# Kernel tuning notes

Hardware: AMD Instinct MI355X
Metric: run time of the kernel (lower is better)

The kernel has to match this reference:

```python
import jax, jax.numpy as jnp
import numpy as np


def _ln(x, g, b, eps=1e-5):
    m = x.mean(-1, keepdims=True)
    v = x.var(-1, keepdims=True)
    return (x - m) / jnp.sqrt(v + eps) * g + b


def setup_inputs() -> dict:
    key = jax.random.key(0)
    ks = jax.random.split(key, 10)
    N, H, E, OUT, L = 4096, 256, 131072, 64, 6
    s = 1.0 / np.sqrt(H)
    return {
        "x": jax.random.normal(ks[0], (N, H), jnp.float32),
        "edge_index": jax.random.randint(ks[1], (2, E), 0, N, jnp.int32),
        "sage_wl": jax.random.normal(ks[2], (L, H, H), jnp.float32) * s,   # lin_l (neighbors, has bias)
        "sage_wr": jax.random.normal(ks[3], (L, H, H), jnp.float32) * s,   # lin_r (root, no bias)
        "sage_bl": jnp.zeros((L, H), jnp.float32),
        "ln_g": jnp.ones((L - 1, H), jnp.float32),
        "ln_b": jnp.zeros((L - 1, H), jnp.float32),
        "conv_w": jax.random.normal(ks[4], (3, H, H, 3), jnp.float32) * (1.0 / np.sqrt(3 * H)),  # [layer,O,I,K]
        "conv_b": jnp.zeros((3, H), jnp.float32),
        "cnorm_g": jnp.ones((3, H), jnp.float32),
        "cnorm_b": jnp.zeros((3, H), jnp.float32),
        "in_proj_w": jax.random.normal(ks[5], (6 * H, 2 * H), jnp.float32) * (1.0 / np.sqrt(2 * H)),
        "in_proj_b": jnp.zeros((6 * H,), jnp.float32),
        "out_proj_w": jax.random.normal(ks[6], (2 * H, 2 * H), jnp.float32) * (1.0 / np.sqrt(2 * H)),
        "out_proj_b": jnp.zeros((2 * H,), jnp.float32),
        "anorm_g": jnp.ones((2 * H,), jnp.float32),
        "anorm_b": jnp.zeros((2 * H,), jnp.float32),
        "fuse_w": jax.random.normal(ks[7], (OUT, 2 * H), jnp.float32) * (1.0 / np.sqrt(2 * H)),
        "fuse_b": jnp.zeros((OUT,), jnp.float32),
    }


def reference(x, edge_index, sage_wl, sage_wr, sage_bl, ln_g, ln_b,
              conv_w, conv_b, cnorm_g, cnorm_b,
              in_proj_w, in_proj_b, out_proj_w, out_proj_b,
              anorm_g, anorm_b, fuse_w, fuse_b):
    # Dropout layers act as identity (eval mode).
    N, H = x.shape
    L = sage_wl.shape[0]
    src, dst = edge_index[0], edge_index[1]
    deg = jax.ops.segment_sum(jnp.ones(src.shape[0], x.dtype), dst, num_segments=N)
    deg = jnp.maximum(deg, 1.0)[:, None]
    h = x
    for i in range(L):
        res = h
        # SAGEConv: mean-aggregate neighbor features (gather/scatter), then two linears
        agg = jax.ops.segment_sum(h[src], dst, num_segments=N) / deg
        h = agg @ sage_wl[i].T + sage_bl[i] + h @ sage_wr[i].T
        if i < L - 1:
            h = _ln(h, ln_g[i], ln_b[i])
        h = jax.nn.relu(h) + res  # residual (shapes always match: in==hidden)
    gnn_out = h                                   # [N, H]

    # CNN branch over the node axis: [1, H, N]
    c = gnn_out.T[None]
    for j in range(3):
        c = jax.lax.conv_general_dilated(c, conv_w[j], (1,), ((1, 1),),
                                         dimension_numbers=("NCH", "OIH", "NCH"))
        c = jax.nn.relu(c + conv_b[j][None, :, None])
        c = _ln(c.transpose(0, 2, 1), cnorm_g[j], cnorm_b[j]).transpose(0, 2, 1)
    cnn_out = c[0].T                              # [N, H]

    fused = jnp.concatenate([gnn_out, cnn_out], axis=1)  # [N, 2H]
    E2 = fused.shape[1]
    heads = 4
    hd = E2 // heads
    qkv = fused @ in_proj_w.T + in_proj_b
    q, k, v = jnp.split(qkv, 3, axis=1)
    split_heads = lambda t: t.reshape(N, heads, hd).transpose(1, 0, 2)  # [h, N, hd]
    q, k, v = split_heads(q), split_heads(k), split_heads(v)
    scores = jnp.einsum("hnd,hmd->hnm", q, k) / np.sqrt(hd).astype(np.float32)
    a = jax.nn.softmax(scores, axis=-1)
    o = jnp.einsum("hnm,hmd->hnd", a, v).transpose(1, 0, 2).reshape(N, E2)
    o = o @ out_proj_w.T + out_proj_b
    o = _ln(o, anorm_g, anorm_b)
    return o @ fuse_w.T + fuse_b                  # [N, out_channels]
```

## Files before the change

### kernel.cpp

```cpp
#include <hip/hip_runtime.h>

#define NN 4096
#define HH 256
#define EE 131072

__device__ __constant__ float LN_EPS = 1e-5f;
#define ATT_SCALE 0.08838834764831845f
#define ATT_SHIFT 30.0f

typedef __attribute__((ext_vector_type(8))) short bf16x8_t;
typedef __attribute__((ext_vector_type(4))) float f32x4_t;

__device__ inline ushort f2b(float f) {
  uint u = __float_as_uint(f);
  uint r = (u + 0x7FFF + ((u >> 16) & 1)) >> 16;
  return (ushort)r;
}

__global__ void hist_kernel(const int* __restrict__ ei, int* __restrict__ cnt) {
  int e = blockIdx.x * blockDim.x + threadIdx.x;
  if (e < EE) atomicAdd(&cnt[ei[EE + e]], 1);
}

__global__ __launch_bounds__(1024) void scan_kernel(int* __restrict__ cnt_cursor,
                                                    int* __restrict__ rowptr,
                                                    float* __restrict__ invdeg) {
  __shared__ int part[1024];
  int t = threadIdx.x;
  int base = t * 4;
  int cs[4];
  int s = 0;
  for (int u = 0; u < 4; ++u) { cs[u] = cnt_cursor[base + u]; s += cs[u]; }
  part[t] = s;
  __syncthreads();
  for (int off = 1; off < 1024; off <<= 1) {
    int add = (t >= off) ? part[t - off] : 0;
    int v = part[t];
    __syncthreads();
    part[t] = v + add;
    __syncthreads();
  }
  int excl = (t > 0) ? part[t - 1] : 0;
  for (int u = 0; u < 4; ++u) {
    rowptr[base + u] = excl;
    cnt_cursor[base + u] = excl;
    invdeg[base + u] = 1.0f / (float)max(cs[u], 1);
    excl += cs[u];
  }
  if (t == 1023) rowptr[NN] = excl;
}

__global__ void fill_kernel(const int* __restrict__ ei, int* __restrict__ cursor,
                            int* __restrict__ col) {
  int e = blockIdx.x * blockDim.x + threadIdx.x;
  if (e < EE) {
    int d = ei[EE + e];
    int p = atomicAdd(&cursor[d], 1);
    col[p] = ei[e];
  }
}

__global__ __launch_bounds__(256) void castw(const float* __restrict__ in,
                                             ushort* __restrict__ out) {
  int i4 = (blockIdx.x * 256 + threadIdx.x) * 4;
  float4 v = *(const float4*)(in + i4);
  ushort4 w;
  w.x = f2b(v.x); w.y = f2b(v.y); w.z = f2b(v.z); w.w = f2b(v.w);
  *(ushort4*)(out + i4) = w;
}

__global__ __launch_bounds__(256) void castconv(const float* __restrict__ w,
                                                ushort* __restrict__ o) {
  int idx = blockIdx.x * 256 + threadIdx.x;
  int j = idx / 196608;
  int rem = idx - j * 196608;
  int oc = rem / 768;
  int kk = rem - oc * 768;
  int ks = kk >> 8, ii = kk & 255;
  o[idx] = f2b(w[j * 196608 + oc * 768 + ii * 3 + ks]);
}

__global__ __launch_bounds__(64) void agg_kernel(const float* __restrict__ h,
                                                 const int* __restrict__ rowptr,
                                                 const int* __restrict__ col,
                                                 const float* __restrict__ invdeg,
                                                 ushort* __restrict__ aggb) {
  int n = blockIdx.x;
  int t = threadIdx.x;
  int s = rowptr[n], e = rowptr[n + 1];
  float4 acc = make_float4(0.f, 0.f, 0.f, 0.f);
  for (int j = s; j < e; ++j) {
    int c = col[j];
    const float4 v = *(const float4*)(h + (size_t)c * HH + t * 4);
    acc.x += v.x; acc.y += v.y; acc.z += v.z; acc.w += v.w;
  }
  float id = invdeg[n];
  ushort4 w;
  w.x = f2b(acc.x * id); w.y = f2b(acc.y * id);
  w.z = f2b(acc.z * id); w.w = f2b(acc.w * id);
  *(ushort4*)(aggb + (size_t)n * HH + t * 4) = w;
}

__global__ __launch_bounds__(256) void gemm_mfma(
    const ushort* __restrict__ A0, const ushort* __restrict__ A1,
    const ushort* __restrict__ B0, const ushort* __restrict__ B1,
    const float* __restrict__ bias, float* __restrict__ Cf, ushort* __restrict__ Cb,
    int M, int Nn, int K, int KHA, int KHB, int relu) {
  __shared__ ushort Alds[64][40];
  __shared__ ushort Blds[128][40];
  int t = threadIdx.x;
  int w = t >> 6, l = t & 63, quad = l >> 4, lr = l & 15;
  int wm = w & 1, wn = w >> 1;
  int m0 = blockIdx.x * 64, n0 = blockIdx.y * 128;
  int sr = t >> 2, sc8 = (t & 3) * 8;
  f32x4_t acc[2][4];
#pragma unroll
  for (int s = 0; s < 2; ++s)
#pragma unroll
    for (int q = 0; q < 4; ++q) acc[s][q] = (f32x4_t){0.f, 0.f, 0.f, 0.f};

  for (int k0 = 0; k0 < K; k0 += 32) {
    int kk = k0 + sc8;
    const ushort* ap = (kk < KHA) ? (A0 + (size_t)(m0 + sr) * KHA + kk)
                                  : (A1 + (size_t)(m0 + sr) * (K - KHA) + (kk - KHA));
    uint4 av = *(const uint4*)ap;
    const ushort* bp0 = (kk < KHB) ? (B0 + (size_t)(n0 + sr) * KHB + kk)
                                   : (B1 + (size_t)(n0 + sr) * (K - KHB) + (kk - KHB));
    uint4 bv0 = *(const uint4*)bp0;
    const ushort* bp1 = (kk < KHB) ? (B0 + (size_t)(n0 + 64 + sr) * KHB + kk)
                                   : (B1 + (size_t)(n0 + 64 + sr) * (K - KHB) + (kk - KHB));
    uint4 bv1 = *(const uint4*)bp1;
    __syncthreads();
    *(uint4*)&Alds[sr][sc8] = av;
    *(uint4*)&Blds[sr][sc8] = bv0;
    *(uint4*)&Blds[64 + sr][sc8] = bv1;
    __syncthreads();
    bf16x8_t af[2], bf[4];
#pragma unroll
    for (int s = 0; s < 2; ++s)
      af[s] = *(const bf16x8_t*)&Alds[wm * 32 + s * 16 + lr][quad * 8];
#pragma unroll
    for (int q = 0; q < 4; ++q)
      bf[q] = *(const bf16x8_t*)&Blds[wn * 64 + q * 16 + lr][quad * 8];
#pragma unroll
    for (int s = 0; s < 2; ++s)
#pragma unroll
      for (int q = 0; q < 4; ++q)
        acc[s][q] = __builtin_amdgcn_mfma_f32_16x16x32_bf16(af[s], bf[q], acc[s][q], 0, 0, 0);
  }
#pragma unroll
  for (int s = 0; s < 2; ++s) {
#pragma unroll
    for (int q = 0; q < 4; ++q) {
      int n = n0 + wn * 64 + q * 16 + lr;
      float bb = bias[n];
#pragma unroll
      for (int r = 0; r < 4; ++r) {
        int m = m0 + wm * 32 + s * 16 + quad * 4 + r;
        float v = acc[s][q][r] + bb;
        if (relu) v = fmaxf(v, 0.f);
        if (Cf) Cf[(size_t)m * Nn + n] = v;
        if (Cb) Cb[(size_t)m * Nn + n] = f2b(v);
      }
    }
  }
}

__global__ __launch_bounds__(256) void gemm_conv_mfma(
    const ushort* __restrict__ Ab, const ushort* __restrict__ B,
    const float* __restrict__ bias, float* __restrict__ Cf) {
  __shared__ ushort Alds[64][40];
  __shared__ ushort Blds[128][40];
  int t = threadIdx.x;
  int w = t >> 6, l = t & 63, quad = l >> 4, lr = l & 15;
  int wm = w & 1, wn = w >> 1;
  int m0 = blockIdx.x * 64, n0 = blockIdx.y * 128;
  int sr = t >> 2, sc8 = (t & 3) * 8;
  f32x4_t acc[2][4];
#pragma unroll
  for (int s = 0; s < 2; ++s)
#pragma unroll
    for (int q = 0; q < 4; ++q) acc[s][q] = (f32x4_t){0.f, 0.f, 0.f, 0.f};

  for (int k0 = 0; k0 < 768; k0 += 32) {
    int kk = k0 + sc8;
    int ks = kk >> 8, ii = kk & 255;
    int nr = m0 + sr + ks - 1;
    uint4 av = make_uint4(0u, 0u, 0u, 0u);
    if (nr >= 0 && nr < NN) av = *(const uint4*)(Ab + (size_t)nr * HH + ii);
    uint4 bv0 = *(const uint4*)(B + (size_t)(n0 + sr) * 768 + kk);
    uint4 bv1 = *(const uint4*)(B + (size_t)(n0 + 64 + sr) * 768 + kk);
    __syncthreads();
    *(uint4*)&Alds[sr][sc8] = av;
    *(uint4*)&Blds[sr][sc8] = bv0;
    *(uint4*)&Blds[64 + sr][sc8] = bv1;
    __syncthreads();
    bf16x8_t af[2], bf[4];
#pragma unroll
    for (int s = 0; s < 2; ++s)
      af[s] = *(const bf16x8_t*)&Alds[wm * 32 + s * 16 + lr][quad * 8];
#pragma unroll
    for (int q = 0; q < 4; ++q)
      bf[q] = *(const bf16x8_t*)&Blds[wn * 64 + q * 16 + lr][quad * 8];
#pragma unroll
    for (int s = 0; s < 2; ++s)
#pragma unroll
      for (int q = 0; q < 4; ++q)
        acc[s][q] = __builtin_amdgcn_mfma_f32_16x16x32_bf16(af[s], bf[q], acc[s][q], 0, 0, 0);
  }
#pragma unroll
  for (int s = 0; s < 2; ++s) {
#pragma unroll
    for (int q = 0; q < 4; ++q) {
      int n = n0 + wn * 64 + q * 16 + lr;
      float bb = bias[n];
#pragma unroll
      for (int r = 0; r < 4; ++r) {
        int m = m0 + wm * 32 + s * 16 + quad * 4 + r;
        Cf[(size_t)m * HH + n] = fmaxf(acc[s][q][r] + bb, 0.f);
      }
    }
  }
}

__global__ __launch_bounds__(256) void gemm_std(
    const float* __restrict__ A0, const float* __restrict__ B0,
    const float* __restrict__ bias, float* __restrict__ C,
    int M, int Nn, int K) {
  __shared__ float As[16][68];
  __shared__ float Bs[16][68];
  int t = threadIdx.x;
  int m0 = blockIdx.x * 64, n0 = blockIdx.y * 64;
  int ty = t >> 4, tx = t & 15;
  int lr = t >> 2, lc4 = (t & 3) * 4;
  float acc[4][4] = {};
  for (int k0 = 0; k0 < K; k0 += 16) {
    int kk = k0 + lc4;
    float4 va = *(const float4*)(A0 + (size_t)(m0 + lr) * K + kk);
    As[lc4 + 0][lr] = va.x; As[lc4 + 1][lr] = va.y;
    As[lc4 + 2][lr] = va.z; As[lc4 + 3][lr] = va.w;
    float4 vb = *(const float4*)(B0 + (size_t)(n0 + lr) * K + kk);
    Bs[lc4 + 0][lr] = vb.x; Bs[lc4 + 1][lr] = vb.y;
    Bs[lc4 + 2][lr] = vb.z; Bs[lc4 + 3][lr] = vb.w;
    __syncthreads();
#pragma unroll
    for (int k = 0; k < 16; ++k) {
      float4 a4 = *(const float4*)&As[k][4 * ty];
      float4 b4 = *(const float4*)&Bs[k][4 * tx];
      float av[4] = {a4.x, a4.y, a4.z, a4.w};
      float bv[4] = {b4.x, b4.y, b4.z, b4.w};
#pragma unroll
      for (int i = 0; i < 4; ++i)
#pragma unroll
        for (int j = 0; j < 4; ++j) acc[i][j] += av[i] * bv[j];
    }
    __syncthreads();
  }
#pragma unroll
  for (int i = 0; i < 4; ++i) {
    int m = m0 + 4 * ty + i;
    float o[4];
#pragma unroll
    for (int j = 0; j < 4; ++j) o[j] = acc[i][j] + bias[n0 + 4 * tx + j];
    float4 o4 = make_float4(o[0], o[1], o[2], o[3]);
    *(float4*)(C + (size_t)m * Nn + n0 + 4 * tx) = o4;
  }
}

__global__ __launch_bounds__(256) void ln_fuse(
    const float* __restrict__ x, const float* __restrict__ g, const float* __restrict__ b,
    const float* __restrict__ res, float* __restrict__ outf, ushort* __restrict__ outb,
    int D, int do_ln, int relu_res) {
  int row = blockIdx.x, t = threadIdx.x;
  int nv = D >> 8;
  float vals[2];
  float s = 0.f, sq = 0.f;
  for (int u = 0; u < nv; ++u) {
    float v = x[(size_t)row * D + t + (u << 8)];
    vals[u] = v; s += v; sq += v * v;
  }
  __shared__ float red[8];
  float m = 0.f, inv = 1.f;
  if (do_ln) {
    for (int off = 32; off >= 1; off >>= 1) {
      s += __shfl_xor(s, off);
      sq += __shfl_xor(sq, off);
    }
    int wid = t >> 6;
    if ((t & 63) == 0) { red[wid] = s; red[4 + wid] = sq; }
    __syncthreads();
    if (t == 0) {
      float S = red[0] + red[1] + red[2] + red[3];
      float Q = red[4] + red[5] + red[6] + red[7];
      float mm = S / D;
      float vv = Q / D - mm * mm;
      red[0] = mm;
      red[1] = rsqrtf(vv + LN_EPS);
    }
    __syncthreads();
    m = red[0]; inv = red[1];
  }
  for (int u = 0; u < nv; ++u) {
    int c = t + (u << 8);
    float y = vals[u];
    if (do_ln) y = (y - m) * inv * g[c] + b[c];
    if (relu_res) y = fmaxf(y, 0.f) + res[(size_t)row * D + c];
    if (outf) outf[(size_t)row * D + c] = y;
    if (outb) outb[(size_t)row * D + c] = f2b(y);
  }
}

__global__ __launch_bounds__(256) void vtrans(const ushort* __restrict__ qkvb,
                                              ushort* __restrict__ Vt) {
  __shared__ ushort tile[32][34];
  int t = threadIdx.x;
  int n0 = blockIdx.x * 32, d0 = blockIdx.y * 32;
  int tx = t & 31, ty = t >> 5;
#pragma unroll
  for (int u = 0; u < 4; ++u) {
    int r = ty + 8 * u;
    tile[r][tx] = qkvb[(size_t)(n0 + r) * 1536 + 1024 + d0 + tx];
  }
  __syncthreads();
#pragma unroll
  for (int u = 0; u < 4; ++u) {
    int dy = ty + 8 * u;
    Vt[(size_t)(d0 + dy) * NN + n0 + tx] = tile[tx][dy];
  }
}

__global__ __launch_bounds__(256) void attn_mfma(const ushort* __restrict__ qkvb,
                                                 const ushort* __restrict__ Vt,
                                                 ushort* __restrict__ Ob) {
  __shared__ ushort Klds[2][64][136];
  __shared__ ushort Vlds[2][128][72];
  __shared__ ushort Plds[4][16][72];

  int t = threadIdx.x;
  int w = t >> 6, l = t & 63;
  int quad = l >> 4, lr = l & 15;
  int half = w >> 1, wq = w & 1;
  int tl = t & 127;
  int head = blockIdx.y;
  int q0 = blockIdx.x * 32;

  bf16x8_t qf[4];
#pragma unroll
  for (int ks = 0; ks < 4; ++ks)
    qf[ks] = *(const bf16x8_t*)(qkvb + (size_t)(q0 + wq * 16 + lr) * 1536 + head * 128 +
                                ks * 32 + quad * 8);

  f32x4_t of[8];
#pragma unroll
  for (int dt = 0; dt < 8; ++dt) of[dt] = (f32x4_t){0.f, 0.f, 0.f, 0.f};
  float den[4] = {0.f, 0.f, 0.f, 0.f};

  for (int ktl = 0; ktl < 32; ++ktl) {
    int k0 = (half * 32 + ktl) * 64;
    __syncthreads();
#pragma unroll
    for (int p = 0; p < 8; ++p) {
      int c0 = tl + p * 128;
      int row = c0 >> 4, c8 = (c0 & 15) * 8;
      *(uint4*)&Klds[half][row][c8] =
          *(const uint4*)(qkvb + (size_t)(k0 + row) * 1536 + 512 + head * 128 + c8);
    }
#pragma unroll
    for (int p = 0; p < 8; ++p) {
      int c0 = tl + p * 128;
      int row = c0 >> 3, kv8 = (c0 & 7) * 8;
      *(uint4*)&Vlds[half][row][kv8] =
          *(const uint4*)(Vt + (size_t)(head * 128 + row) * NN + k0 + kv8);
    }
    __syncthreads();

    f32x4_t sf[4];
#pragma unroll
    for (int ct = 0; ct < 4; ++ct) sf[ct] = (f32x4_t){0.f, 0.f, 0.f, 0.f};
#pragma unroll
    for (int ks = 0; ks < 4; ++ks) {
#pragma unroll
      for (int ct = 0; ct < 4; ++ct) {
        bf16x8_t kf = *(const bf16x8_t*)&Klds[half][ct * 16 + lr][ks * 32 + quad * 8];
        sf[ct] = __builtin_amdgcn_mfma_f32_16x16x32_bf16(qf[ks], kf, sf[ct], 0, 0, 0);
      }
    }

    float rs[4] = {0.f, 0.f, 0.f, 0.f};
#pragma unroll
    for (int ct = 0; ct < 4; ++ct) {
#pragma unroll
      for (int r = 0; r < 4; ++r) {
        float e = __expf(sf[ct][r] * ATT_SCALE - ATT_SHIFT);
        Plds[w][quad * 4 + r][ct * 16 + lr] = f2b(e);
        rs[r] += e;
      }
    }
#pragma unroll
    for (int mask = 1; mask < 16; mask <<= 1) {
#pragma unroll
      for (int r = 0; r < 4; ++r) rs[r] += __shfl_xor(rs[r], mask);
    }
#pragma unroll
    for (int r = 0; r < 4; ++r) den[r] += rs[r];

#pragma unroll
    for (int ks2 = 0; ks2 < 2; ++ks2) {
      bf16x8_t pf = *(const bf16x8_t*)&Plds[w][lr][ks2 * 32 + quad * 8];
#pragma unroll
      for (int dt = 0; dt < 8; ++dt) {
        bf16x8_t vf = *(const bf16x8_t*)&Vlds[half][dt * 16 + lr][ks2 * 32 + quad * 8];
        of[dt] = __builtin_amdgcn_mfma_f32_16x16x32_bf16(pf, vf, of[dt], 0, 0, 0);
      }
    }
  }

  __syncthreads();
  float* smemO = (float*)&Klds[0][0][0];
  float* smemD = (float*)&Vlds[0][0][0];
  if (half == 1) {
#pragma unroll
    for (int dt = 0; dt < 8; ++dt)
#pragma unroll
      for (int r = 0; r < 4; ++r)
        smemO[(size_t)(wq * 16 + quad * 4 + r) * 128 + dt * 16 + lr] = of[dt][r];
    if (lr == 0) {
#pragma unroll
      for (int r = 0; r < 4; ++r) smemD[wq * 16 + quad * 4 + r] = den[r];
    }
  }
  __syncthreads();
  if (half == 0) {
    float inv[4];
#pragma unroll
    for (int r = 0; r < 4; ++r)
      inv[r] = 1.0f / (den[r] + smemD[wq * 16 + quad * 4 + r]);
#pragma unroll
    for (int dt = 0; dt < 8; ++dt) {
#pragma unroll
      for (int r = 0; r < 4; ++r) {
        int row = q0 + wq * 16 + quad * 4 + r;
        float v = of[dt][r] + smemO[(size_t)(wq * 16 + quad * 4 + r) * 128 + dt * 16 + lr];
        Ob[(size_t)row * 512 + head * 128 + dt * 16 + lr] = f2b(v * inv[r]);
      }
    }
  }
}

extern "C" void kernel_launch(void* const* d_in, const int* in_sizes, int n_in,
                              void* d_out, int out_size, void* d_ws, size_t ws_size,
                              hipStream_t stream) {
  const float* x          = (const float*)d_in[0];
  const int*   ei         = (const int*)d_in[1];
  const float* sage_wl    = (const float*)d_in[2];
  const float* sage_wr    = (const float*)d_in[3];
  const float* sage_bl    = (const float*)d_in[4];
  const float* ln_g       = (const float*)d_in[5];
  const float* ln_b       = (const float*)d_in[6];
  const float* conv_w     = (const float*)d_in[7];
  const float* conv_b     = (const float*)d_in[8];
  const float* cnorm_g    = (const float*)d_in[9];
  const float* cnorm_b    = (const float*)d_in[10];
  const float* in_proj_w  = (const float*)d_in[11];
  const float* in_proj_b  = (const float*)d_in[12];
  const float* out_proj_w = (const float*)d_in[13];
  const float* out_proj_b = (const float*)d_in[14];
  const float* anorm_g    = (const float*)d_in[15];
  const float* anorm_b    = (const float*)d_in[16];
  const float* fuse_w     = (const float*)d_in[17];
  const float* fuse_b     = (const float*)d_in[18];
  float* out = (float*)d_out;

  char* ws = (char*)d_ws;
  const size_t MB = 1 << 20;
  int*    rowptr = (int*)(ws + 0);
  int*    cnt    = (int*)(ws + 65536);
  int*    col    = (int*)(ws + 131072);
  float*  invdeg = (float*)(ws + 786432);
  float*  h    = (float*)(ws + 1 * MB);
  ushort* hb   = (ushort*)(ws + 5 * MB);
  ushort* aggb = (ushort*)(ws + 7 * MB);
  float*  tmp  = (float*)(ws + 9 * MB);
  ushort* c0b  = (ushort*)(ws + 13 * MB);
  ushort* c1b  = (ushort*)(ws + 15 * MB);
  ushort* qkvb = (ushort*)(ws + 17 * MB);
  float*  op   = (float*)(ws + 17 * MB);
  ushort* Vt   = (ushort*)(ws + 29 * MB);
  ushort* aob  = (ushort*)(ws + 33 * MB);
  ushort* wlb  = (ushort*)(ws + 37 * MB);
  ushort* wrb  = (ushort*)(ws + 37 * MB + 786432);
  ushort* cvb  = (ushort*)(ws + 37 * MB + 1572864);
  ushort* ipb  = (ushort*)(ws + 37 * MB + 2752512);
  ushort* opb  = (ushort*)(ws + 37 * MB + 4325376);

  castw<<<(6 * 256 * 256) / 1024, 256, 0, stream>>>(sage_wl, wlb);
  castw<<<(6 * 256 * 256) / 1024, 256, 0, stream>>>(sage_wr, wrb);
  castconv<<<(3 * 256 * 768) / 256, 256, 0, stream>>>(conv_w, cvb);
  castw<<<(1536 * 512) / 1024, 256, 0, stream>>>(in_proj_w, ipb);
  castw<<<(512 * 512) / 1024, 256, 0, stream>>>(out_proj_w, opb);

  hipMemsetAsync(cnt, 0, NN * sizeof(int), stream);
  hist_kernel<<<EE / 256, 256, 0, stream>>>(ei, cnt);
  scan_kernel<<<1, 1024, 0, stream>>>(cnt, rowptr, invdeg);
  fill_kernel<<<EE / 256, 256, 0, stream>>>(ei, cnt, col);
  hipMemcpyAsync(h, x, (size_t)NN * HH * sizeof(float), hipMemcpyDeviceToDevice, stream);
  castw<<<(NN * HH) / 1024, 256, 0, stream>>>(x, hb);

  for (int i = 0; i < 6; ++i) {
    agg_kernel<<<NN, 64, 0, stream>>>(h, rowptr, col, invdeg, aggb);
    gemm_mfma<<<dim3(64, 2), 256, 0, stream>>>(
        aggb, hb, wlb + (size_t)i * HH * HH, wrb + (size_t)i * HH * HH,
        sage_bl + i * HH, tmp, nullptr, NN, HH, 512, 256, 256, 0);
    int do_ln = (i < 5) ? 1 : 0;
    const float* gp = do_ln ? (ln_g + i * HH) : ln_g;
    const float* bp = do_ln ? (ln_b + i * HH) : ln_b;
    ln_fuse<<<NN, 256, 0, stream>>>(tmp, gp, bp, h, h, hb, HH, do_ln, 1);
  }

  const ushort* cin = hb;
  ushort* couts[3] = {c0b, c1b, c0b};
  for (int j = 0; j < 3; ++j) {
    gemm_conv_mfma<<<dim3(64, 2), 256, 0, stream>>>(
        cin, cvb + (size_t)j * HH * 768, conv_b + j * HH, tmp);
    ln_fuse<<<NN, 256, 0, stream>>>(tmp, cnorm_g + j * HH, cnorm_b + j * HH,
                                    nullptr, nullptr, couts[j], HH, 1, 0);
    cin = couts[j];
  }

  gemm_mfma<<<dim3(64, 12), 256, 0, stream>>>(
      hb, c0b, ipb, nullptr, in_proj_b, nullptr, qkvb, NN, 1536, 512, 256, 1536 * 0 + 512, 0);
  vtrans<<<dim3(NN / 32, 512 / 32), 256, 0, stream>>>(qkvb, Vt);
  attn_mfma<<<dim3(NN / 32, 4), 256, 0, stream>>>(qkvb, Vt, aob);

  gemm_mfma<<<dim3(64, 4), 256, 0, stream>>>(
      aob, nullptr, opb, nullptr, out_proj_b, op, nullptr, NN, 512, 512, 512, 512, 0);
  ln_fuse<<<NN, 256, 0, stream>>>(op, anorm_g, anorm_b, nullptr, op, nullptr, 512, 1, 0);
  gemm_std<<<dim3(64, 1), 256, 0, stream>>>(op, fuse_w, fuse_b, out, NN, 64, 512);
}
```

Measured before the change: 581.5 us.

## Restructure attention kernel into per-wave KV split with register-prefetched tiles

The attention kernel now has each of its four waves process all 32 query rows against its own quarter of the keys, using private LDS tiles. This removes the block-wide __syncthreads inside the KV loop. The next K/V tile is prefetched into registers while the current one is computed. K tiles are XOR-swizzled in LDS to avoid bank conflicts, and V is pre-tiled by vtrans into a contiguous [head][ktile][d][32] layout. The price is a 4-way partial-sum reduction through shared memory at the end, more registers and about 74KB of LDS per block, which may limit occupancy.

```diff
diff --git a/kernel.cpp b/kernel.cpp
--- a/kernel.cpp
+++ b/kernel.cpp
@@ -311,7 +311,7 @@
 }
 
 __global__ __launch_bounds__(256) void vtrans(const ushort* __restrict__ qkvb,
-                                              ushort* __restrict__ Vt) {
+                                              ushort* __restrict__ VtT) {
   __shared__ ushort tile[32][34];
   int t = threadIdx.x;
   int n0 = blockIdx.x * 32, d0 = blockIdx.y * 32;
@@ -322,128 +322,166 @@
     tile[r][tx] = qkvb[(size_t)(n0 + r) * 1536 + 1024 + d0 + tx];
   }
   __syncthreads();
+  int kb = n0 >> 5;
 #pragma unroll
   for (int u = 0; u < 4; ++u) {
-    int dy = ty + 8 * u;
-    Vt[(size_t)(d0 + dy) * NN + n0 + tx] = tile[tx][dy];
-  }
-}
-
-__global__ __launch_bounds__(256) void attn_mfma(const ushort* __restrict__ qkvb,
-                                                 const ushort* __restrict__ Vt,
-                                                 ushort* __restrict__ Ob) {
-  __shared__ ushort Klds[2][64][136];
-  __shared__ ushort Vlds[2][128][72];
-  __shared__ ushort Plds[4][16][72];
-
+    int dg = d0 + ty + 8 * u;
+    int head = dg >> 7, dl = dg & 127;
+    VtT[((((size_t)head * 128 + kb) * 128 + dl) << 5) + tx] = tile[tx][ty + 8 * u];
+  }
+}
+
+__global__ __launch_bounds__(256, 2) void attn_mfma(const ushort* __restrict__ qkvb,
+                                                    const ushort* __restrict__ VtT,
+                                                    ushort* __restrict__ Ob) {
+  __shared__ __align__(16) char smem[75776];
   int t = threadIdx.x;
   int w = t >> 6, l = t & 63;
   int quad = l >> 4, lr = l & 15;
-  int half = w >> 1, wq = w & 1;
-  int tl = t & 127;
   int head = blockIdx.y;
   int q0 = blockIdx.x * 32;
 
-  bf16x8_t qf[4];
-#pragma unroll
-  for (int ks = 0; ks < 4; ++ks)
-    qf[ks] = *(const bf16x8_t*)(qkvb + (size_t)(q0 + wq * 16 + lr) * 1536 + head * 128 +
-                                ks * 32 + quad * 8);
-
-  f32x4_t of[8];
-#pragma unroll
-  for (int dt = 0; dt < 8; ++dt) of[dt] = (f32x4_t){0.f, 0.f, 0.f, 0.f};
-  float den[4] = {0.f, 0.f, 0.f, 0.f};
-
-  for (int ktl = 0; ktl < 32; ++ktl) {
-    int k0 = (half * 32 + ktl) * 64;
-    __syncthreads();
+  ushort* Kl = (ushort*)(smem) + w * 4096;
+  ushort* Vl = (ushort*)(smem + 32768) + w * 4096;
+  ushort* Pl = (ushort*)(smem + 65536) + w * 1280;
+
+  bf16x8_t qf[2][4];
+#pragma unroll
+  for (int s = 0; s < 2; ++s)
+#pragma unroll
+    for (int ks = 0; ks < 4; ++ks)
+      qf[s][ks] = *(const bf16x8_t*)(qkvb + (size_t)(q0 + s * 16 + lr) * 1536 +
+                                     head * 128 + ks * 32 + quad * 8);
+
+  f32x4_t of[2][8];
+#pragma unroll
+  for (int s = 0; s < 2; ++s)
+#pragma unroll
+    for (int dt = 0; dt < 8; ++dt) of[s][dt] = (f32x4_t){0.f, 0.f, 0.f, 0.f};
+  float den[2][4] = {{0.f, 0.f, 0.f, 0.f}, {0.f, 0.f, 0.f, 0.f}};
+
+  const int tile0 = w * 32;
+  const ushort* kgbase = qkvb + 512 + head * 128;
+  const ushort* vgbase = VtT + ((size_t)head * 128) * 4096;
+
+  uint4 kr[8], vr[8];
+  {
+    int k0 = tile0 * 32;
 #pragma unroll
     for (int p = 0; p < 8; ++p) {
-      int c0 = tl + p * 128;
-      int row = c0 >> 4, c8 = (c0 & 15) * 8;
-      *(uint4*)&Klds[half][row][c8] =
-          *(const uint4*)(qkvb + (size_t)(k0 + row) * 1536 + 512 + head * 128 + c8);
+      int c0 = l + p * 64;
+      int row = c0 >> 4, cc = c0 & 15;
+      kr[p] = *(const uint4*)(kgbase + (size_t)(k0 + row) * 1536 + cc * 8);
+      vr[p] = *(const uint4*)(vgbase + (size_t)tile0 * 4096 + c0 * 8);
     }
 #pragma unroll
     for (int p = 0; p < 8; ++p) {
-      int c0 = tl + p * 128;
-      int row = c0 >> 3, kv8 = (c0 & 7) * 8;
-      *(uint4*)&Vlds[half][row][kv8] =
-          *(const uint4*)(Vt + (size_t)(head * 128 + row) * NN + k0 + kv8);
-    }
-    __syncthreads();
-
-    f32x4_t sf[4];
-#pragma unroll
-    for (int ct = 0; ct < 4; ++ct) sf[ct] = (f32x4_t){0.f, 0.f, 0.f, 0.f};
+      int c0 = l + p * 64;
+      int row = c0 >> 4, cc = c0 & 15;
+      *(uint4*)&Kl[row * 128 + ((cc ^ (row & 7)) * 8)] = kr[p];
+      *(uint4*)&Vl[c0 * 8] = vr[p];
+    }
+  }
+
+  for (int tt = 0; tt < 32; ++tt) {
+    int kt = tile0 + tt;
+    if (tt < 31) {
+      int k0n = (kt + 1) * 32;
+#pragma unroll
+      for (int p = 0; p < 8; ++p) {
+        int c0 = l + p * 64;
+        int row = c0 >> 4, cc = c0 & 15;
+        kr[p] = *(const uint4*)(kgbase + (size_t)(k0n + row) * 1536 + cc * 8);
+        vr[p] = *(const uint4*)(vgbase + (size_t)(kt + 1) * 4096 + c0 * 8);
+      }
+    }
+
+    f32x4_t sf[2][2];
+#pragma unroll
+    for (int s = 0; s < 2; ++s)
+#pragma unroll
+      for (int ct = 0; ct < 2; ++ct) sf[s][ct] = (f32x4_t){0.f, 0.f, 0.f, 0.f};
 #pragma unroll
     for (int ks = 0; ks < 4; ++ks) {
 #pragma unroll
-      for (int ct = 0; ct < 4; ++ct) {
-        bf16x8_t kf = *(const bf16x8_t*)&Klds[half][ct * 16 + lr][ks * 32 + quad * 8];
-        sf[ct] = __builtin_amdgcn_mfma_f32_16x16x32_bf16(qf[ks], kf, sf[ct], 0, 0, 0);
+      for (int ct = 0; ct < 2; ++ct) {
+        int krow = ct * 16 + lr;
+        bf16x8_t kf =
+            *(const bf16x8_t*)&Kl[krow * 128 + (((ks * 4 + quad) ^ (krow & 7)) * 8)];
+#pragma unroll
+        for (int s = 0; s < 2; ++s)
+          sf[s][ct] = __builtin_amdgcn_mfma_f32_16x16x32_bf16(qf[s][ks], kf, sf[s][ct], 0, 0, 0);
       }
     }
 
-    float rs[4] = {0.f, 0.f, 0.f, 0.f};
-#pragma unroll
-    for (int ct = 0; ct < 4; ++ct) {
-#pragma unroll
-      for (int r = 0; r < 4; ++r) {
-        float e = __expf(sf[ct][r] * ATT_SCALE - ATT_SHIFT);
-        Plds[w][quad * 4 + r][ct * 16 + lr] = f2b(e);
-        rs[r] += e;
+    float rs[2][4] = {{0.f, 0.f, 0.f, 0.f}, {0.f, 0.f, 0.f, 0.f}};
+#pragma unroll
+    for (int s = 0; s < 2; ++s)
+#pragma unroll
+      for (int ct = 0; ct < 2; ++ct)
+#pragma unroll
+        for (int r = 0; r < 4; ++r) {
+          float e = __expf(sf[s][ct][r] * ATT_SCALE - ATT_SHIFT);
+          Pl[(s * 16 + quad * 4 + r) * 40 + ct * 16 + lr] = f2b(e);
+          rs[s][r] += e;
+        }
+#pragma unroll
+    for (int mask = 1; mask < 16; mask <<= 1)
+#pragma unroll
+      for (int s = 0; s < 2; ++s)
+#pragma unroll
+        for (int r = 0; r < 4; ++r) rs[s][r] += __shfl_xor(rs[s][r], mask);
+#pragma unroll
+    for (int s = 0; s < 2; ++s)
+#pragma unroll
+      for (int r = 0; r < 4; ++r) den[s][r] += rs[s][r];
+
+#pragma unroll
+    for (int s = 0; s < 2; ++s) {
+      bf16x8_t pf = *(const bf16x8_t*)&Pl[(s * 16 + lr) * 40 + quad * 8];
+#pragma unroll
+      for (int dt = 0; dt < 8; ++dt) {
+        bf16x8_t vf = *(const bf16x8_t*)&Vl[(dt * 16 + lr) * 32 + quad * 8];
+        of[s][dt] = __builtin_amdgcn_mfma_f32_16x16x32_bf16(pf, vf, of[s][dt], 0, 0, 0);
       }
     }
-#pragma unroll
-    for (int mask = 1; mask < 16; mask <<= 1) {
-#pragma unroll
-      for (int r = 0; r < 4; ++r) rs[r] += __shfl_xor(rs[r], mask);
-    }
-#pragma unroll
-    for (int r = 0; r < 4; ++r) den[r] += rs[r];
-
-#pragma unroll
-    for (int ks2 = 0; ks2 < 2; ++ks2) {
-      bf16x8_t pf = *(const bf16x8_t*)&Plds[w][lr][ks2 * 32 + quad * 8];
-#pragma unroll
-      for (int dt = 0; dt < 8; ++dt) {
-        bf16x8_t vf = *(const bf16x8_t*)&Vlds[half][dt * 16 + lr][ks2 * 32 + quad * 8];
-        of[dt] = __builtin_amdgcn_mfma_f32_16x16x32_bf16(pf, vf, of[dt], 0, 0, 0);
+
+    if (tt < 31) {
+#pragma unroll
+      for (int p = 0; p < 8; ++p) {
+        int c0 = l + p * 64;
+        int row = c0 >> 4, cc = c0 & 15;
+        *(uint4*)&Kl[row * 128 + ((cc ^ (row & 7)) * 8)] = kr[p];
+        *(uint4*)&Vl[c0 * 8] = vr[p];
       }
     }
   }
 
   __syncthreads();
-  float* smemO = (float*)&Klds[0][0][0];
-  float* smemD = (float*)&Vlds[0][0][0];
-  if (half == 1) {
+  float* Osum = (float*)smem;
+  float* Dsum = (float*)(smem + 65536);
+#pragma unroll
+  for (int s = 0; s < 2; ++s)
 #pragma unroll
     for (int dt = 0; dt < 8; ++dt)
 #pragma unroll
       for (int r = 0; r < 4; ++r)
-        smemO[(size_t)(wq * 16 + quad * 4 + r) * 128 + dt * 16 + lr] = of[dt][r];
-    if (lr == 0) {
-#pragma unroll
-      for (int r = 0; r < 4; ++r) smemD[wq * 16 + quad * 4 + r] = den[r];
-    }
+        Osum[w * 4096 + (s * 16 + quad * 4 + r) * 128 + dt * 16 + lr] = of[s][dt][r];
+  if (lr == 0) {
+#pragma unroll
+    for (int s = 0; s < 2; ++s)
+#pragma unroll
+      for (int r = 0; r < 4; ++r) Dsum[w * 32 + s * 16 + quad * 4 + r] = den[s][r];
   }
   __syncthreads();
-  if (half == 0) {
-    float inv[4];
-#pragma unroll
-    for (int r = 0; r < 4; ++r)
-      inv[r] = 1.0f / (den[r] + smemD[wq * 16 + quad * 4 + r]);
-#pragma unroll
-    for (int dt = 0; dt < 8; ++dt) {
-#pragma unroll
-      for (int r = 0; r < 4; ++r) {
-        int row = q0 + wq * 16 + quad * 4 + r;
-        float v = of[dt][r] + smemO[(size_t)(wq * 16 + quad * 4 + r) * 128 + dt * 16 + lr];
-        Ob[(size_t)row * 512 + head * 128 + dt * 16 + lr] = f2b(v * inv[r]);
-      }
-    }
+#pragma unroll
+  for (int e = 0; e < 16; ++e) {
+    int idx = l + e * 64;
+    int row = w * 8 + (idx >> 7), col = idx & 127;
+    float o = Osum[row * 128 + col] + Osum[4096 + row * 128 + col] +
+              Osum[8192 + row * 128 + col] + Osum[12288 + row * 128 + col];
+    float dn = Dsum[row] + Dsum[32 + row] + Dsum[64 + row] + Dsum[96 + row];
+    Ob[(size_t)(q0 + row) * 512 + head * 128 + col] = f2b(o / dn);
   }
 }
 
```

Result: slower. 653.4 us (+12.4%).
